# Optimization experiments

Hardware: AMD Instinct MI355X
Metric: run time of the kernel (lower is better)

## Reference

```python
import jax, jax.numpy as jnp
import numpy as np

B, Cin, Cout = 2, 32, 16
D, H, W = 48, 64, 128
K = 3
EPS = 1e-5  # BatchNorm3d default eps


def setup_inputs() -> dict:
    key = jax.random.key(0)
    ks = jax.random.split(key, 6)
    return {
        "x": jax.random.normal(ks[0], (B, Cin, D, H, W), jnp.float32),
        "weight": jax.random.normal(ks[1], (Cout, Cin, K, K, K), jnp.float32) * 0.05,
        "gamma": jax.random.uniform(ks[2], (Cout,), jnp.float32, minval=0.5, maxval=1.5),
        "beta": jax.random.normal(ks[3], (Cout,), jnp.float32) * 0.1,
        "running_mean": jax.random.normal(ks[4], (Cout,), jnp.float32) * 0.1,
        "running_var": jax.random.uniform(ks[5], (Cout,), jnp.float32, minval=0.5, maxval=1.5),
    }


def _binarize(v):
    # forward: sign(v) in {-1, 0, +1}; backward (STE): hardtanh grad (pass-through on |v|<=1)
    clipped = jnp.clip(v, -1.0, 1.0)
    return clipped + jax.lax.stop_gradient(jnp.sign(v) - clipped)


def reference(x, weight, gamma, beta, running_mean, running_var):
    b, c, d, h, w = x.shape
    # trilinear upsample, scale (1,2,2), align_corners=False (half-pixel centers)
    x = jax.image.resize(x, (b, c, d, 2 * h, 2 * w), method="trilinear")
    # binarize activations and weights; XNOR-style per-output-channel scale alpha = mean|W|
    xb = _binarize(x)
    alpha = jnp.mean(jnp.abs(weight), axis=(1, 2, 3, 4), keepdims=True)  # [Cout,1,1,1,1]
    wb = _binarize(weight) * alpha
    y = jax.lax.conv_general_dilated(
        xb, wb,
        window_strides=(1, 1, 1),
        padding=[(1, 1), (1, 1), (1, 1)],
        dimension_numbers=("NCDHW", "OIDHW", "NCDHW"),
    )  # [B, Cout, D, 2H, 2W]
    # fused BatchNorm3d (inference form) + ReLU
    inv = gamma / jnp.sqrt(running_var + EPS)
    shift = beta - running_mean * inv
    y = y * inv[None, :, None, None, None] + shift[None, :, None, None, None]
    return jax.nn.relu(y)
```

## Files before the change

### kernel.cpp

```cpp
#include <hip/hip_runtime.h>
#include <hip/hip_bf16.h>
#include <stdint.h>

#define BB   2
#define CIN  32
#define COUT 16
#define DD   48
#define HIN  64
#define WIN  128
#define H2   128
#define W2   256
#define PLANE_WORDS (H2 * W2)

__global__ __launch_bounds__(256) void ibc3d_prep16(
    const float* __restrict__ wgt, const float* __restrict__ gamma,
    const float* __restrict__ beta, const float* __restrict__ rmean,
    const float* __restrict__ rvar, uint32_t* __restrict__ bw,
    float* __restrict__ scale, float* __restrict__ shift)
{
    __shared__ float sw[CIN * 27];
    __shared__ double sp[256];

    int co  = blockIdx.x;
    int tid = threadIdx.x;
    const float* wslice = wgt + (size_t)co * (CIN * 27);

    double p = 0.0;
    for (int i = tid; i < CIN * 27; i += 256) {
        float v = wslice[i];
        sw[i] = v;
        p += fabs((double)v);
    }
    sp[tid] = p;
    __syncthreads();

#pragma unroll
    for (int s = 128; s > 0; s >>= 1) {
        if (tid < s) sp[tid] += sp[tid + s];
        __syncthreads();
    }

    if (tid < 27) {
        int tap = tid;
        uint32_t word = 0;
#pragma unroll
        for (int ci = 0; ci < CIN; ++ci)
            word |= (sw[ci * 27 + tap] > 0.0f ? 1u : 0u) << ci;
        bw[tap * 16 + co] = word;
    }
    if (tid == 0) {
        float alpha = (float)(sp[0] / (double)(CIN * 27));
        float inv = gamma[co] / sqrtf(rvar[co] + 1e-5f);
        scale[co] = alpha * inv;
        shift[co] = beta[co] - rmean[co] * inv;
    }
}

__device__ __forceinline__ uint32_t pack_word(const float* __restrict__ x,
                                              int b, int d, int h2, int w2)
{
    int m = h2 >> 1, dh = h2 & 1;
    int n = w2 >> 1, dwp = w2 & 1;
    int rA = m + dh - 1;
    int rB = rA + 1;
    double wA = dh ? 0.75 : 0.25;
    double wB = 1.0 - wA;
    rA = rA < 0 ? 0 : rA;
    rB = rB > (HIN - 1) ? (HIN - 1) : rB;
    int cA = n + dwp - 1;
    int cB = cA + 1;
    double wC = dwp ? 0.75 : 0.25;
    double wD = 1.0 - wC;
    cA = cA < 0 ? 0 : cA;
    cB = cB > (WIN - 1) ? (WIN - 1) : cB;

    const float* xp = x + ((size_t)b * CIN * DD + d) * (HIN * WIN);
    int oA = rA * WIN, oB = rB * WIN;
    uint32_t word = 0;
    for (int ci = 0; ci < CIN; ++ci) {
        const float* xc = xp + (size_t)ci * (DD * HIN * WIN);
        float a0 = xc[oA + cA], a1 = xc[oA + cB];
        float b0 = xc[oB + cA], b1 = xc[oB + cB];
        double t0 = wA * (double)a0 + wB * (double)b0;
        double t1 = wA * (double)a1 + wB * (double)b1;
        double v  = wC * t0 + wD * t1;
        word |= (v >= 0.0 ? 1u : 0u) << ci;
    }
    return word;
}

__global__ __launch_bounds__(256) void ibc3d_packr8(
    const float* __restrict__ x, uint32_t* __restrict__ bx,
    int b_start, int nplanes)
{
    int per = gridDim.x >> 3;
    int bid = (blockIdx.x & 7) * per + (blockIdx.x >> 3);
    int idx = bid * 256 + threadIdx.x;
    int j  = idx & 31;
    int h2 = (idx >> 5) & (H2 - 1);
    int pl = idx >> 12;
    if (pl >= nplanes) return;
    int d  = pl % DD;
    int b  = b_start + pl / DD;

    int m = h2 >> 1, q = h2 & 1;
    int rT = q ? m : (m > 0 ? m - 1 : 0);
    int rB = q ? (m < HIN - 1 ? m + 1 : HIN - 1) : m;
    float wT = q ? 0.75f : 0.25f;
    float wB = 1.0f - wT;

    int c0 = 4 * j;
    int cl = c0 >= 2 ? c0 - 2 : 0;
    int cr = (c0 + 4 <= WIN - 2) ? c0 + 4 : WIN - 2;

    const float* xp = x + ((size_t)b * CIN * DD + d) * (HIN * WIN);
    int oT = rT * WIN, oB2 = rB * WIN;

    uint32_t w[8];
#pragma unroll
    for (int k = 0; k < 8; ++k) w[k] = 0u;

#pragma unroll 2
    for (int ci = 0; ci < CIN; ++ci) {
        const float* xc = xp + (size_t)ci * (DD * HIN * WIN);
        float cT[6], cB[6];
        {
            const float* rowT = xc + oT;
            float2 L = *(const float2*)(rowT + cl);
            float4 M = *(const float4*)(rowT + c0);
            float2 R = *(const float2*)(rowT + cr);
            cT[0] = (j > 0)  ? L.y : L.x;
            cT[1] = M.x; cT[2] = M.y; cT[3] = M.z; cT[4] = M.w;
            cT[5] = (j < 31) ? R.x : R.y;
        }
        {
            const float* rowB = xc + oB2;
            float2 L = *(const float2*)(rowB + cl);
            float4 M = *(const float4*)(rowB + c0);
            float2 R = *(const float2*)(rowB + cr);
            cB[0] = (j > 0)  ? L.y : L.x;
            cB[1] = M.x; cB[2] = M.y; cB[3] = M.z; cB[4] = M.w;
            cB[5] = (j < 31) ? R.x : R.y;
        }

        float v[8];
#pragma unroll
        for (int t = 0; t < 4; ++t) {
            float uT0 = 0.25f * cT[t]     + 0.75f * cT[t + 1];
            float uT1 = 0.75f * cT[t + 1] + 0.25f * cT[t + 2];
            float uB0 = 0.25f * cB[t]     + 0.75f * cB[t + 1];
            float uB1 = 0.75f * cB[t + 1] + 0.25f * cB[t + 2];
            v[2 * t]     = wT * uT0 + wB * uB0;
            v[2 * t + 1] = wT * uT1 + wB * uB1;
        }

        float amin = 3.4e38f;
#pragma unroll
        for (int k = 0; k < 8; ++k)
            amin = fminf(amin, fabsf(v[k]));

        if (__builtin_expect(amin < 1e-5f, 0)) {
            double dwT = (double)wT, dwB = 1.0 - (double)wT;
#pragma unroll
            for (int t = 0; t < 4; ++t) {
                double eT0 = 0.25 * (double)cT[t]     + 0.75 * (double)cT[t + 1];
                double eT1 = 0.75 * (double)cT[t + 1] + 0.25 * (double)cT[t + 2];
                double eB0 = 0.25 * (double)cB[t]     + 0.75 * (double)cB[t + 1];
                double eB1 = 0.75 * (double)cB[t + 1] + 0.25 * (double)cB[t + 2];
                uint32_t s0 = (dwT * eT0 + dwB * eB0) >= 0.0;
                uint32_t s1 = (dwT * eT1 + dwB * eB1) >= 0.0;
                w[2 * t]     |= s0 << ci;
                w[2 * t + 1] |= s1 << ci;
            }
        } else {
#pragma unroll
            for (int k = 0; k < 8; ++k)
                w[k] |= (v[k] >= 0.0f ? 1u : 0u) << ci;
        }
    }

    size_t base = (size_t)pl * PLANE_WORDS + (size_t)h2 * W2 + 8 * j;
    *(uint4*)(bx + base)     = make_uint4(w[0], w[1], w[2], w[3]);
    *(uint4*)(bx + base + 4) = make_uint4(w[4], w[5], w[6], w[7]);
}

__global__ __launch_bounds__(256) void ibc3d_conv3(
    const uint32_t* __restrict__ bx, const uint32_t* __restrict__ bwg,
    const float* __restrict__ scaleg, const float* __restrict__ shiftg,
    float* __restrict__ out, int b_start)
{
    int bid   = blockIdx.x;
    int h2    = bid & (H2 - 1);
    int plane = bid >> 7;
    int d     = plane % DD;
    int b     = b_start + plane / DD;
    int w2    = threadIdx.x;

    int acc[16];
#pragma unroll
    for (int c = 0; c < 16; ++c) acc[c] = 0;

#pragma unroll
    for (int kd = 0; kd < 3; ++kd) {
        int dd = d + kd - 1;
        if (dd < 0 || dd >= DD) continue;
        const uint32_t* bxp = bx + (size_t)(plane + kd - 1) * PLANE_WORDS;
#pragma unroll
        for (int kh = 0; kh < 3; ++kh) {
            int hh = h2 + kh - 1;
            if (hh < 0 || hh >= H2) continue;
            const uint32_t* brow = bxp + hh * W2;
#pragma unroll
            for (int kw = 0; kw < 3; ++kw) {
                int ww = w2 + kw - 1;
                if (ww >= 0 && ww < W2) {
                    uint32_t word = brow[ww];
                    int tap = kd * 9 + kh * 3 + kw;
#pragma unroll
                    for (int co = 0; co < 16; ++co)
                        acc[co] += __popc(word ^ bwg[tap * 16 + co]);
                }
            }
        }
    }

    int nd = 1 + (d > 0)  + (d < DD - 1);
    int nh = 1 + (h2 > 0) + (h2 < H2 - 1);
    int nw = 1 + (w2 > 0) + (w2 < W2 - 1);
    float base = 32.0f * (float)(nd * nh * nw);

    size_t obase = (((size_t)(b * COUT) * DD + d) * H2 + h2) * W2 + w2;
#pragma unroll
    for (int co = 0; co < 16; ++co) {
        float y = (base - 2.0f * (float)acc[co]) * scaleg[co] + shiftg[co];
        y = y > 0.0f ? y : 0.0f;
        out[obase + (size_t)co * (DD * H2 * W2)] = y;
    }
}

__global__ __launch_bounds__(256) void ibc3d_fused(
    const float* __restrict__ x, const float* __restrict__ wgt,
    const float* __restrict__ gamma, const float* __restrict__ beta,
    const float* __restrict__ rmean, const float* __restrict__ rvar,
    float* __restrict__ out)
{
    __shared__ uint32_t sbw[27 * 16];
    __shared__ float sscale[16];
    __shared__ float sshift[16];
    __shared__ uint32_t sw[3][10][264];

    int tid = threadIdx.x;
    for (int t = tid; t < 27 * 16; t += 256) {
        int tap = t >> 4, co = t & 15;
        uint32_t word = 0;
        for (int ci = 0; ci < CIN; ++ci) {
            float v = wgt[(co * CIN + ci) * 27 + tap];
            word |= (v > 0.0f ? 1u : 0u) << ci;
        }
        sbw[t] = word;
    }
    if (tid < 16) {
        int co = tid;
        double s = 0.0;
        for (int i = 0; i < CIN * 27; ++i)
            s += fabs((double)wgt[co * CIN * 27 + i]);
        float alpha = (float)(s / (double)(CIN * 27));
        float inv = gamma[co] / sqrtf(rvar[co] + 1e-5f);
        sscale[co] = alpha * inv;
        sshift[co] = beta[co] - rmean[co] * inv;
    }

    int bid = blockIdx.x;
    int hq  = bid & 15;
    int r   = bid >> 4;
    int b   = r / DD;
    int d   = r % DD;
    int h2base = hq * 8;

    for (int i = tid; i < 3 * 10 * 258; i += 256) {
        int kd  = i / 2580;
        int rem = i - kd * 2580;
        int ri  = rem / 258;
        int ciw = rem - ri * 258;
        int dd = d + kd - 1;
        int h2 = h2base - 1 + ri;
        int w2 = ciw - 1;
        uint32_t word = 0;
        if (dd >= 0 && dd < DD && h2 >= 0 && h2 < H2 && w2 >= 0 && w2 < W2)
            word = pack_word(x, b, dd, h2, w2);
        sw[kd][ri][ciw] = word;
    }
    __syncthreads();

    int w2 = tid;
    for (int p = 0; p < 8; ++p) {
        int h2 = h2base + p;
        int acc[16];
#pragma unroll
        for (int c = 0; c < 16; ++c) acc[c] = 0;
        int nv = 0;
        for (int kd = 0; kd < 3; ++kd) {
            int dd = d + kd - 1;
            if (dd < 0 || dd >= DD) continue;
            for (int kh = 0; kh < 3; ++kh) {
                int hh = h2 + kh - 1;
                if (hh < 0 || hh >= H2) continue;
                for (int kw = 0; kw < 3; ++kw) {
                    int ww = w2 + kw - 1;
                    if (ww < 0 || ww >= W2) continue;
                    uint32_t word = sw[kd][p + kh][w2 + kw];
                    nv += 1;
                    int tap = kd * 9 + kh * 3 + kw;
#pragma unroll
                    for (int co = 0; co < 16; ++co)
                        acc[co] += __popc(word ^ sbw[tap * 16 + co]);
                }
            }
        }
        float base = 32.0f * (float)nv;
#pragma unroll
        for (int co = 0; co < 16; ++co) {
            float y = (base - 2.0f * (float)acc[co]) * sscale[co] + sshift[co];
            y = y > 0.0f ? y : 0.0f;
            size_t oidx = (((size_t)(b * COUT + co) * DD + d) * H2 + h2) * W2 + w2;
            out[oidx] = y;
        }
    }
}

extern "C" void kernel_launch(void* const* d_in, const int* in_sizes, int n_in,
                              void* d_out, int out_size, void* d_ws, size_t ws_size,
                              hipStream_t stream)
{
    (void)in_sizes; (void)n_in; (void)out_size;
    const float* x     = (const float*)d_in[0];
    const float* wgt   = (const float*)d_in[1];
    const float* gamma = (const float*)d_in[2];
    const float* beta  = (const float*)d_in[3];
    const float* rmean = (const float*)d_in[4];
    const float* rvar  = (const float*)d_in[5];
    float* out = (float*)d_out;

    const size_t HDR = 4096;
    const size_t bx_full = (size_t)BB * DD * PLANE_WORDS * 4;
    const size_t bx_half = (size_t)DD * PLANE_WORDS * 4;

    if (d_ws != nullptr && ws_size >= HDR + bx_full) {
        uint8_t* ws = (uint8_t*)d_ws;
        uint32_t* bw    = (uint32_t*)ws;
        float*    scale = (float*)(ws + 2048);
        float*    shift = (float*)(ws + 2112);
        uint32_t* bx    = (uint32_t*)(ws + HDR);
        ibc3d_prep16<<<16, 256, 0, stream>>>(wgt, gamma, beta, rmean, rvar, bw, scale, shift);
        int nplanes = BB * DD;
        ibc3d_packr8<<<nplanes * 16, 256, 0, stream>>>(x, bx, 0, nplanes);
        ibc3d_conv3<<<nplanes * H2, 256, 0, stream>>>(bx, bw, scale, shift, out, 0);
    } else if (d_ws != nullptr && ws_size >= HDR + bx_half) {
        uint8_t* ws = (uint8_t*)d_ws;
        uint32_t* bw    = (uint32_t*)ws;
        float*    scale = (float*)(ws + 2048);
        float*    shift = (float*)(ws + 2112);
        uint32_t* bx    = (uint32_t*)(ws + HDR);
        ibc3d_prep16<<<16, 256, 0, stream>>>(wgt, gamma, beta, rmean, rvar, bw, scale, shift);
        for (int b = 0; b < BB; ++b) {
            ibc3d_packr8<<<DD * 16, 256, 0, stream>>>(x, bx, b, DD);
            ibc3d_conv3<<<DD * H2, 256, 0, stream>>>(bx, bw, scale, shift, out, b);
        }
    } else {
        ibc3d_fused<<<BB * DD * (H2 / 8), 256, 0, stream>>>(
            x, wgt, gamma, beta, rmean, rvar, out);
    }
}
```

Measured before the change: 143.0 us.

## Replace XNOR-popcount conv with int8 MFMA over zero-padded signed activations

Activations are now packed as signed int8 (+1/-1) into a spatially zero-padded buffer. Weights become int8 {-1,0,+1} matrices laid out for the 16x16x64 i8 MFMA, and the 27-tap binary convolution runs as matrix-core accumulations instead of per-thread XOR/popcount loops. Zero padding removes the boundary branches and the border-count correction. The trade is 8x larger intermediate storage (32 bytes per site versus 4), an extra kernel phase that zeroes the padding, and dependence on a larger workspace, which falls back to the fused path when the workspace is too small.

After: 240.7 us, median of 2. +68.3%, slower.

```diff
diff --git a/kernel.cpp b/kernel.cpp
--- a/kernel.cpp
+++ b/kernel.cpp
@@ -10,49 +10,247 @@
 #define WIN  128
 #define H2   128
 #define W2   256
-#define PLANE_WORDS (H2 * W2)
-
-__global__ __launch_bounds__(256) void ibc3d_prep16(
+
+#define WP   258
+#define HP   130
+#define PDP  (WP * HP)
+#define PB   (PDP * 50)
+#define NSITES ((size_t)PB * BB)
+
+#define NPAD_R1 134160
+#define NPAD_R2 49536
+#define NPAD_R3 24576
+#define NPAD   (NPAD_R1 + NPAD_R2 + NPAD_R3)
+
+typedef int v4i __attribute__((ext_vector_type(4)));
+
+__global__ __launch_bounds__(256) void ibc3d_prepB(
     const float* __restrict__ wgt, const float* __restrict__ gamma,
     const float* __restrict__ beta, const float* __restrict__ rmean,
-    const float* __restrict__ rvar, uint32_t* __restrict__ bw,
-    float* __restrict__ scale, float* __restrict__ shift)
-{
-    __shared__ float sw[CIN * 27];
+    const float* __restrict__ rvar, uint8_t* __restrict__ Bmat,
+    float* __restrict__ scale, float* __restrict__ shift,
+    uint8_t* __restrict__ xb)
+{
     __shared__ double sp[256];
-
-    int co  = blockIdx.x;
+    int bid = blockIdx.x, tid = threadIdx.x;
+
+    if (bid < 16) {
+        int co = bid;
+        const float* wsl = wgt + (size_t)co * (CIN * 27);
+
+        if (tid < 56) {
+            int p  = tid >> 2;
+            int lq = tid & 3;
+            int l  = lq * 16 + co;
+            int tap = (l >= 32) ? (2 * p + 1) : (2 * p);
+            uint32_t dw[4] = {0u, 0u, 0u, 0u};
+            if (tap < 27) {
+                int cib = ((l >> 4) & 1) * 16;
+                for (int jj = 0; jj < 16; ++jj) {
+                    float w = wsl[(cib + jj) * 27 + tap];
+                    uint32_t sb = w > 0.f ? 0x01u : (w < 0.f ? 0xFFu : 0x00u);
+                    dw[jj >> 2] |= sb << ((jj & 3) * 8);
+                }
+            }
+            *(uint4*)(Bmat + ((size_t)p * 64 + l) * 16) =
+                make_uint4(dw[0], dw[1], dw[2], dw[3]);
+        }
+
+        double s = 0.0;
+        for (int i = tid; i < CIN * 27; i += 256) s += fabs((double)wsl[i]);
+        sp[tid] = s;
+        __syncthreads();
+#pragma unroll
+        for (int st = 128; st > 0; st >>= 1) {
+            if (tid < st) sp[tid] += sp[tid + st];
+            __syncthreads();
+        }
+        if (tid == 0) {
+            float alpha = (float)(sp[0] / (double)(CIN * 27));
+            float inv = gamma[co] / sqrtf(rvar[co] + 1e-5f);
+            scale[co] = alpha * inv;
+            shift[co] = beta[co] - rmean[co] * inv;
+        }
+    } else {
+        int i = (bid - 16) * 256 + tid;
+        if (i >= NPAD) return;
+        size_t site;
+        if (i < NPAD_R1) {
+            int bq = i / 67080; int m = i - bq * 67080;
+            int ds = m / PDP;   int r2 = m - ds * PDP;
+            int hp = r2 / WP,   wp = r2 % WP;
+            site = (size_t)bq * PB + (size_t)(ds ? 49 : 0) * PDP + hp * WP + wp;
+        } else if (i < NPAD_R1 + NPAD_R2) {
+            int i2 = i - NPAD_R1;
+            int bq = i2 / 24768; int m = i2 - bq * 24768;
+            int dp = 1 + m / 516; int r2 = m - (dp - 1) * 516;
+            int hp = (r2 / WP) ? 129 : 0; int wp = r2 % WP;
+            site = (size_t)bq * PB + (size_t)dp * PDP + hp * WP + wp;
+        } else {
+            int i3 = i - NPAD_R1 - NPAD_R2;
+            int bq = i3 / 12288; int m = i3 - bq * 12288;
+            int dp = 1 + m / 256; int r2 = m & 255;
+            int hp = 1 + (r2 >> 1); int wp = (r2 & 1) ? 257 : 0;
+            site = (size_t)bq * PB + (size_t)dp * PDP + hp * WP + wp;
+        }
+        uint8_t* pz = xb + site * 32;
+        *(uint4*)pz        = make_uint4(0u, 0u, 0u, 0u);
+        *(uint4*)(pz + 16) = make_uint4(0u, 0u, 0u, 0u);
+    }
+}
+
+__global__ __launch_bounds__(256) void ibc3d_packi8(
+    const float* __restrict__ x, uint8_t* __restrict__ xb)
+{
+    int idx = blockIdx.x * 256 + threadIdx.x;
+    int j  = idx & 31;
+    int q  = (idx >> 5) & 3;
+    int h2 = (idx >> 7) & 127;
+    int pl = idx >> 14;
+    int d = pl % DD, b = pl / DD;
+
+    int m = h2 >> 1, qq = h2 & 1;
+    int rT = qq ? m : (m > 0 ? m - 1 : 0);
+    int rB = qq ? (m < HIN - 1 ? m + 1 : HIN - 1) : m;
+    float wT = qq ? 0.75f : 0.25f;
+    float wB = 1.0f - wT;
+
+    int c0 = 4 * j;
+    int cl = c0 >= 2 ? c0 - 2 : 0;
+    int cr = (c0 + 4 <= WIN - 2) ? c0 + 4 : WIN - 2;
+
+    const float* xp = x + ((size_t)b * CIN * DD + d) * (HIN * WIN);
+    int oT = rT * WIN, oB2 = rB * WIN;
+
+    uint32_t d0[8], d1[8];
+#pragma unroll
+    for (int k = 0; k < 8; ++k) { d0[k] = 0u; d1[k] = 0u; }
+
+    for (int c = 0; c < 8; ++c) {
+        int ci = q * 8 + c;
+        const float* xc = xp + (size_t)ci * (DD * HIN * WIN);
+        float cT[6], cB[6];
+        {
+            const float* rowT = xc + oT;
+            float2 L = *(const float2*)(rowT + cl);
+            float4 M = *(const float4*)(rowT + c0);
+            float2 R = *(const float2*)(rowT + cr);
+            cT[0] = (j > 0)  ? L.y : L.x;
+            cT[1] = M.x; cT[2] = M.y; cT[3] = M.z; cT[4] = M.w;
+            cT[5] = (j < 31) ? R.x : R.y;
+        }
+        {
+            const float* rowB = xc + oB2;
+            float2 L = *(const float2*)(rowB + cl);
+            float4 M = *(const float4*)(rowB + c0);
+            float2 R = *(const float2*)(rowB + cr);
+            cB[0] = (j > 0)  ? L.y : L.x;
+            cB[1] = M.x; cB[2] = M.y; cB[3] = M.z; cB[4] = M.w;
+            cB[5] = (j < 31) ? R.x : R.y;
+        }
+
+        float v[8];
+#pragma unroll
+        for (int t = 0; t < 4; ++t) {
+            float uT0 = 0.25f * cT[t]     + 0.75f * cT[t + 1];
+            float uT1 = 0.75f * cT[t + 1] + 0.25f * cT[t + 2];
+            float uB0 = 0.25f * cB[t]     + 0.75f * cB[t + 1];
+            float uB1 = 0.75f * cB[t + 1] + 0.25f * cB[t + 2];
+            v[2 * t]     = wT * uT0 + wB * uB0;
+            v[2 * t + 1] = wT * uT1 + wB * uB1;
+        }
+
+        float amin = 3.4e38f;
+#pragma unroll
+        for (int k = 0; k < 8; ++k) amin = fminf(amin, fabsf(v[k]));
+
+        uint32_t sb[8];
+        if (__builtin_expect(amin < 1e-5f, 0)) {
+            double dwT = (double)wT, dwB = 1.0 - (double)wT;
+#pragma unroll
+            for (int t = 0; t < 4; ++t) {
+                double eT0 = 0.25 * (double)cT[t]     + 0.75 * (double)cT[t + 1];
+                double eT1 = 0.75 * (double)cT[t + 1] + 0.25 * (double)cT[t + 2];
+                double eB0 = 0.25 * (double)cB[t]     + 0.75 * (double)cB[t + 1];
+                double eB1 = 0.75 * (double)cB[t + 1] + 0.25 * (double)cB[t + 2];
+                sb[2 * t]     = (dwT * eT0 + dwB * eB0) >= 0.0 ? 0x01u : 0xFFu;
+                sb[2 * t + 1] = (dwT * eT1 + dwB * eB1) >= 0.0 ? 0x01u : 0xFFu;
+            }
+        } else {
+#pragma unroll
+            for (int k = 0; k < 8; ++k) sb[k] = v[k] >= 0.f ? 0x01u : 0xFFu;
+        }
+
+        if (c < 4) {
+#pragma unroll
+            for (int k = 0; k < 8; ++k) d0[k] |= sb[k] << (c * 8);
+        } else {
+#pragma unroll
+            for (int k = 0; k < 8; ++k) d1[k] |= sb[k] << ((c - 4) * 8);
+        }
+    }
+
+    size_t base = (size_t)b * PB + (size_t)(d + 1) * PDP +
+                  (size_t)(h2 + 1) * WP + 1 + j * 8;
+#pragma unroll
+    for (int k = 0; k < 8; ++k)
+        *(uint2*)(xb + (base + k) * 32 + q * 8) = make_uint2(d0[k], d1[k]);
+}
+
+__global__ __launch_bounds__(256) void ibc3d_convmf(
+    const uint8_t* __restrict__ xb, const uint8_t* __restrict__ Bmat,
+    const float* __restrict__ scaleg, const float* __restrict__ shiftg,
+    float* __restrict__ out)
+{
+    int bid = blockIdx.x;
+    int h2 = bid & 127;
+    int pl = bid >> 7;
+    int b = pl / DD, d = pl % DD;
     int tid = threadIdx.x;
-    const float* wslice = wgt + (size_t)co * (CIN * 27);
-
-    double p = 0.0;
-    for (int i = tid; i < CIN * 27; i += 256) {
-        float v = wslice[i];
-        sw[i] = v;
-        p += fabs((double)v);
-    }
-    sp[tid] = p;
-    __syncthreads();
-
-#pragma unroll
-    for (int s = 128; s > 0; s >>= 1) {
-        if (tid < s) sp[tid] += sp[tid + s];
-        __syncthreads();
-    }
-
-    if (tid < 27) {
-        int tap = tid;
-        uint32_t word = 0;
-#pragma unroll
-        for (int ci = 0; ci < CIN; ++ci)
-            word |= (sw[ci * 27 + tap] > 0.0f ? 1u : 0u) << ci;
-        bw[tap * 16 + co] = word;
-    }
-    if (tid == 0) {
-        float alpha = (float)(sp[0] / (double)(CIN * 27));
-        float inv = gamma[co] / sqrtf(rvar[co] + 1e-5f);
-        scale[co] = alpha * inv;
-        shift[co] = beta[co] - rmean[co] * inv;
+    int l = tid & 63, wid = tid >> 6;
+    int ls = l & 15;
+    bool hi = l >= 32;
+    int ci0 = ((l >> 4) & 1) * 16;
+
+    v4i bf[14];
+#pragma unroll
+    for (int p = 0; p < 14; ++p)
+        bf[p] = *(const v4i*)(Bmat + ((size_t)p * 64 + l) * 16);
+
+    size_t base = (size_t)b * PB + (size_t)(d + 1) * PDP +
+                  (size_t)(h2 + 1) * WP + 1;
+
+    v4i acc[4];
+#pragma unroll
+    for (int g = 0; g < 4; ++g) acc[g] = (v4i){0, 0, 0, 0};
+
+#pragma unroll
+    for (int p = 0; p < 14; ++p) {
+        const int t0 = 2 * p;
+        const int t1 = (2 * p + 1 < 27) ? (2 * p + 1) : 26;
+        const int off0 = (t0 / 9 - 1) * PDP + ((t0 % 9) / 3 - 1) * WP + (t0 % 3 - 1);
+        const int off1 = (t1 / 9 - 1) * PDP + ((t1 % 9) / 3 - 1) * WP + (t1 % 3 - 1);
+        int offs = hi ? off1 : off0;
+#pragma unroll
+        for (int g = 0; g < 4; ++g) {
+            size_t s = base + (size_t)((wid * 4 + g) * 16 + ls);
+            const v4i a = *(const v4i*)(xb + (s + offs) * 32 + ci0);
+            acc[g] = __builtin_amdgcn_mfma_i32_16x16x64_i8(a, bf[p], acc[g], 0, 0, 0);
+        }
+    }
+
+    int co = ls;
+    float sc = scaleg[co], sh = shiftg[co];
+    size_t obase = (((size_t)(b * COUT + co) * DD + d) * H2 + h2) * W2;
+#pragma unroll
+    for (int g = 0; g < 4; ++g) {
+        int grp = wid * 4 + g;
+#pragma unroll
+        for (int r = 0; r < 4; ++r) {
+            int w2 = grp * 16 + ((l >> 4) << 2) + r;
+            float y = (float)acc[g][r] * sc + sh;
+            out[obase + w2] = y > 0.f ? y : 0.f;
+        }
     }
 }
 
@@ -89,155 +287,6 @@
     return word;
 }
 
-__global__ __launch_bounds__(256) void ibc3d_packr8(
-    const float* __restrict__ x, uint32_t* __restrict__ bx,
-    int b_start, int nplanes)
-{
-    int per = gridDim.x >> 3;
-    int bid = (blockIdx.x & 7) * per + (blockIdx.x >> 3);
-    int idx = bid * 256 + threadIdx.x;
-    int j  = idx & 31;
-    int h2 = (idx >> 5) & (H2 - 1);
-    int pl = idx >> 12;
-    if (pl >= nplanes) return;
-    int d  = pl % DD;
-    int b  = b_start + pl / DD;
-
-    int m = h2 >> 1, q = h2 & 1;
-    int rT = q ? m : (m > 0 ? m - 1 : 0);
-    int rB = q ? (m < HIN - 1 ? m + 1 : HIN - 1) : m;
-    float wT = q ? 0.75f : 0.25f;
-    float wB = 1.0f - wT;
-
-    int c0 = 4 * j;
-    int cl = c0 >= 2 ? c0 - 2 : 0;
-    int cr = (c0 + 4 <= WIN - 2) ? c0 + 4 : WIN - 2;
-
-    const float* xp = x + ((size_t)b * CIN * DD + d) * (HIN * WIN);
-    int oT = rT * WIN, oB2 = rB * WIN;
-
-    uint32_t w[8];
-#pragma unroll
-    for (int k = 0; k < 8; ++k) w[k] = 0u;
-
-#pragma unroll 2
-    for (int ci = 0; ci < CIN; ++ci) {
-        const float* xc = xp + (size_t)ci * (DD * HIN * WIN);
-        float cT[6], cB[6];
-        {
-            const float* rowT = xc + oT;
-            float2 L = *(const float2*)(rowT + cl);
-            float4 M = *(const float4*)(rowT + c0);
-            float2 R = *(const float2*)(rowT + cr);
-            cT[0] = (j > 0)  ? L.y : L.x;
-            cT[1] = M.x; cT[2] = M.y; cT[3] = M.z; cT[4] = M.w;
-            cT[5] = (j < 31) ? R.x : R.y;
-        }
-        {
-            const float* rowB = xc + oB2;
-            float2 L = *(const float2*)(rowB + cl);
-            float4 M = *(const float4*)(rowB + c0);
-            float2 R = *(const float2*)(rowB + cr);
-            cB[0] = (j > 0)  ? L.y : L.x;
-            cB[1] = M.x; cB[2] = M.y; cB[3] = M.z; cB[4] = M.w;
-            cB[5] = (j < 31) ? R.x : R.y;
-        }
-
-        float v[8];
-#pragma unroll
-        for (int t = 0; t < 4; ++t) {
-            float uT0 = 0.25f * cT[t]     + 0.75f * cT[t + 1];
-            float uT1 = 0.75f * cT[t + 1] + 0.25f * cT[t + 2];
-            float uB0 = 0.25f * cB[t]     + 0.75f * cB[t + 1];
-            float uB1 = 0.75f * cB[t + 1] + 0.25f * cB[t + 2];
-            v[2 * t]     = wT * uT0 + wB * uB0;
-            v[2 * t + 1] = wT * uT1 + wB * uB1;
-        }
-
-        float amin = 3.4e38f;
-#pragma unroll
-        for (int k = 0; k < 8; ++k)
-            amin = fminf(amin, fabsf(v[k]));
-
-        if (__builtin_expect(amin < 1e-5f, 0)) {
-            double dwT = (double)wT, dwB = 1.0 - (double)wT;
-#pragma unroll
-            for (int t = 0; t < 4; ++t) {
-                double eT0 = 0.25 * (double)cT[t]     + 0.75 * (double)cT[t + 1];
-                double eT1 = 0.75 * (double)cT[t + 1] + 0.25 * (double)cT[t + 2];
-                double eB0 = 0.25 * (double)cB[t]     + 0.75 * (double)cB[t + 1];
-                double eB1 = 0.75 * (double)cB[t + 1] + 0.25 * (double)cB[t + 2];
-                uint32_t s0 = (dwT * eT0 + dwB * eB0) >= 0.0;
-                uint32_t s1 = (dwT * eT1 + dwB * eB1) >= 0.0;
-                w[2 * t]     |= s0 << ci;
-                w[2 * t + 1] |= s1 << ci;
-            }
-        } else {
-#pragma unroll
-            for (int k = 0; k < 8; ++k)
-                w[k] |= (v[k] >= 0.0f ? 1u : 0u) << ci;
-        }
-    }
-
-    size_t base = (size_t)pl * PLANE_WORDS + (size_t)h2 * W2 + 8 * j;
-    *(uint4*)(bx + base)     = make_uint4(w[0], w[1], w[2], w[3]);
-    *(uint4*)(bx + base + 4) = make_uint4(w[4], w[5], w[6], w[7]);
-}
-
-__global__ __launch_bounds__(256) void ibc3d_conv3(
-    const uint32_t* __restrict__ bx, const uint32_t* __restrict__ bwg,
-    const float* __restrict__ scaleg, const float* __restrict__ shiftg,
-    float* __restrict__ out, int b_start)
-{
-    int bid   = blockIdx.x;
-    int h2    = bid & (H2 - 1);
-    int plane = bid >> 7;
-    int d     = plane % DD;
-    int b     = b_start + plane / DD;
-    int w2    = threadIdx.x;
-
-    int acc[16];
-#pragma unroll
-    for (int c = 0; c < 16; ++c) acc[c] = 0;
-
-#pragma unroll
-    for (int kd = 0; kd < 3; ++kd) {
-        int dd = d + kd - 1;
-        if (dd < 0 || dd >= DD) continue;
-        const uint32_t* bxp = bx + (size_t)(plane + kd - 1) * PLANE_WORDS;
-#pragma unroll
-        for (int kh = 0; kh < 3; ++kh) {
-            int hh = h2 + kh - 1;
-            if (hh < 0 || hh >= H2) continue;
-            const uint32_t* brow = bxp + hh * W2;
-#pragma unroll
-            for (int kw = 0; kw < 3; ++kw) {
-                int ww = w2 + kw - 1;
-                if (ww >= 0 && ww < W2) {
-                    uint32_t word = brow[ww];
-                    int tap = kd * 9 + kh * 3 + kw;
-#pragma unroll
-                    for (int co = 0; co < 16; ++co)
-                        acc[co] += __popc(word ^ bwg[tap * 16 + co]);
-                }
-            }
-        }
-    }
-
-    int nd = 1 + (d > 0)  + (d < DD - 1);
-    int nh = 1 + (h2 > 0) + (h2 < H2 - 1);
-    int nw = 1 + (w2 > 0) + (w2 < W2 - 1);
-    float base = 32.0f * (float)(nd * nh * nw);
-
-    size_t obase = (((size_t)(b * COUT) * DD + d) * H2 + h2) * W2 + w2;
-#pragma unroll
-    for (int co = 0; co < 16; ++co) {
-        float y = (base - 2.0f * (float)acc[co]) * scaleg[co] + shiftg[co];
-        y = y > 0.0f ? y : 0.0f;
-        out[obase + (size_t)co * (DD * H2 * W2)] = y;
-    }
-}
-
 __global__ __launch_bounds__(256) void ibc3d_fused(
     const float* __restrict__ x, const float* __restrict__ wgt,
     const float* __restrict__ gamma, const float* __restrict__ beta,
@@ -341,31 +390,21 @@
     const float* rvar  = (const float*)d_in[5];
     float* out = (float*)d_out;
 
-    const size_t HDR = 4096;
-    const size_t bx_full = (size_t)BB * DD * PLANE_WORDS * 4;
-    const size_t bx_half = (size_t)DD * PLANE_WORDS * 4;
-
-    if (d_ws != nullptr && ws_size >= HDR + bx_full) {
-        uint8_t* ws = (uint8_t*)d_ws;
-        uint32_t* bw    = (uint32_t*)ws;
-        float*    scale = (float*)(ws + 2048);
-        float*    shift = (float*)(ws + 2112);
-        uint32_t* bx    = (uint32_t*)(ws + HDR);
-        ibc3d_prep16<<<16, 256, 0, stream>>>(wgt, gamma, beta, rmean, rvar, bw, scale, shift);
-        int nplanes = BB * DD;
-        ibc3d_packr8<<<nplanes * 16, 256, 0, stream>>>(x, bx, 0, nplanes);
-        ibc3d_conv3<<<nplanes * H2, 256, 0, stream>>>(bx, bw, scale, shift, out, 0);
-    } else if (d_ws != nullptr && ws_size >= HDR + bx_half) {
-        uint8_t* ws = (uint8_t*)d_ws;
-        uint32_t* bw    = (uint32_t*)ws;
-        float*    scale = (float*)(ws + 2048);
-        float*    shift = (float*)(ws + 2112);
-        uint32_t* bx    = (uint32_t*)(ws + HDR);
-        ibc3d_prep16<<<16, 256, 0, stream>>>(wgt, gamma, beta, rmean, rvar, bw, scale, shift);
-        for (int b = 0; b < BB; ++b) {
-            ibc3d_packr8<<<DD * 16, 256, 0, stream>>>(x, bx, b, DD);
-            ibc3d_conv3<<<DD * H2, 256, 0, stream>>>(bx, bw, scale, shift, out, b);
-        }
+    const size_t XBOFF = 32768;
+    const size_t need = XBOFF + NSITES * 32;
+
+    if (d_ws != nullptr && ws_size >= need) {
+        uint8_t* ws    = (uint8_t*)d_ws;
+        uint8_t* Bmat  = ws;
+        float*   scale = (float*)(ws + 16384);
+        float*   shift = (float*)(ws + 16448);
+        uint8_t* xb    = ws + XBOFF;
+
+        int zblocks = 16 + (NPAD + 255) / 256;
+        ibc3d_prepB<<<zblocks, 256, 0, stream>>>(wgt, gamma, beta, rmean, rvar,
+                                                 Bmat, scale, shift, xb);
+        ibc3d_packi8<<<6144, 256, 0, stream>>>(x, xb);
+        ibc3d_convmf<<<BB * DD * H2, 256, 0, stream>>>(xb, Bmat, scale, shift, out);
     } else {
         ibc3d_fused<<<BB * DD * (H2 / 8), 256, 0, stream>>>(
             x, wgt, gamma, beta, rmean, rvar, out);
```
